# Performance work log

Measured on AMD Instinct MI355X. Metric: run time of the kernel, lower is better.

## Reference

```python
import jax, jax.numpy as jnp
import numpy as np

HEADS = 16
PHI = (1.0 + np.sqrt(5.0)) / 2.0


def setup_inputs() -> dict:
    key = jax.random.key(0)
    k1, k2, k3, k4 = jax.random.split(key, 4)
    B, L, D = 2, 2048, 1024
    x = jax.random.normal(k1, (B, L, D), dtype=jnp.float32)
    # nn.Linear(dim, 3*dim, bias=False): store as [D, 3D] for x @ W
    w_qkv = jax.random.normal(k2, (D, 3 * D), dtype=jnp.float32) * (D ** -0.5)
    w_proj = jax.random.normal(k3, (D, D), dtype=jnp.float32) * (D ** -0.5)
    b_proj = jax.random.normal(k4, (D,), dtype=jnp.float32) * 0.01
    return {"x": x, "w_qkv": w_qkv, "w_proj": w_proj, "b_proj": b_proj}


def phi_bias(L):
    # pos[i] = (i * phi) mod 1 ; bias = log(exp(-|pos_i - pos_j|) + 1e-8)
    pos = (jnp.arange(L, dtype=jnp.float32) * PHI) % 1.0
    dist = jnp.abs(pos[:, None] - pos[None, :])  # [L, L]
    return jnp.log(jnp.exp(-dist) + 1e-8)


def reference(x, w_qkv, w_proj, b_proj):
    B, L, D = x.shape
    H = HEADS
    Dh = D // H
    scale = Dh ** -0.5
    qkv = (x @ w_qkv).reshape(B, L, 3, H, Dh)
    q = jnp.transpose(qkv[:, :, 0], (0, 2, 1, 3))  # [B, H, L, Dh]
    k = jnp.transpose(qkv[:, :, 1], (0, 2, 1, 3))
    v = jnp.transpose(qkv[:, :, 2], (0, 2, 1, 3))
    attn = jnp.einsum("bhid,bhjd->bhij", q, k) * scale  # [B, H, L, L]
    attn = attn + phi_bias(L)[None, None]  # additive phi-distance bias
    attn = jax.nn.softmax(attn, axis=-1)
    out = jnp.einsum("bhij,bhjd->bhid", attn, v)  # [B, H, L, Dh]
    out = jnp.transpose(out, (0, 2, 1, 3)).reshape(B, L, D)
    return out @ w_proj + b_proj
```

## Files before the change

### kernel.cpp

```cpp
#include <hip/hip_runtime.h>
#include <math.h>


typedef _Float16 f16;
typedef _Float16 f16x4 __attribute__((ext_vector_type(4)));
typedef _Float16 f16x8 __attribute__((ext_vector_type(8)));
typedef float f32x4 __attribute__((ext_vector_type(4)));

#define MFMA32(a, b, c) __builtin_amdgcn_mfma_f32_16x16x32_f16(a, b, c, 0, 0, 0)

static constexpr int Bsz = 2, Lseq = 2048, Dm = 1024, H = 16, Dh = 64;
static constexpr int Mtot = Bsz * Lseq;
static constexpr int NQKV = 3 * Dm;
static constexpr float PHI_F = 1.61803398874989484820f;
static constexpr float LOG2E = 1.44269504088896f;
static constexpr float QS = 0.125f * LOG2E;
static constexpr float CSTEP = 0.55417527999932633f;

__device__ __forceinline__ void load16_to_lds(const f16* g, f16* l) {
  __builtin_amdgcn_global_load_lds(
      (const __attribute__((address_space(1))) unsigned int*)g,
      (__attribute__((address_space(3))) unsigned int*)l, 16, 0, 0);
}

__global__ __launch_bounds__(256) void cast_f32_f16(const float* __restrict__ in,
                                                    f16* __restrict__ out, int n) {
  int i = (blockIdx.x * 256 + threadIdx.x) * 4;
  if (i < n) {
    float4 v = *reinterpret_cast<const float4*>(in + i);
    f16 t[4] = {(f16)v.x, (f16)v.y, (f16)v.z, (f16)v.w};
    *reinterpret_cast<uint2*>(out + i) = *reinterpret_cast<uint2*>(t);
  }
}

__global__ __launch_bounds__(256) void transpose_cast(const float* __restrict__ in,
                                                      f16* __restrict__ out,
                                                      int K, int N) {
  __shared__ float tile[32][33];
  int n0 = blockIdx.x * 32, k0 = blockIdx.y * 32;
  int tx = threadIdx.x & 31, ty = threadIdx.x >> 5;
#pragma unroll
  for (int r = 0; r < 32; r += 8)
    tile[ty + r][tx] = in[(size_t)(k0 + ty + r) * N + n0 + tx];
  __syncthreads();
#pragma unroll
  for (int r = 0; r < 32; r += 8)
    out[(size_t)(n0 + ty + r) * K + k0 + tx] = (f16)tile[tx][ty + r];
}

__global__ __launch_bounds__(256) void v_transpose(const f16* __restrict__ in,
                                                   f16* __restrict__ out) {
  __shared__ f16 td[64][68];
  int bh = blockIdx.y, l0 = blockIdx.x * 64;
  int tid = threadIdx.x;
  const f16* src = in + (size_t)bh * Lseq * Dh;
#pragma unroll
  for (int c = tid; c < 512; c += 256) {
    int row = c >> 3, col = (c & 7) * 8;
    uint4 v = *reinterpret_cast<const uint4*>(src + (size_t)(l0 + row) * Dh + col);
    f16 tmp[8];
    *reinterpret_cast<uint4*>(tmp) = v;
#pragma unroll
    for (int j = 0; j < 8; j++) td[col + j][row] = tmp[j];
  }
  __syncthreads();
  f16* dst = out + (size_t)bh * Dh * Lseq;
#pragma unroll
  for (int c = tid; c < 512; c += 256) {
    int d = c >> 3, co = c & 7;
    int jh = co >> 2, qd = co & 3;
    f16 tmp[8];
#pragma unroll
    for (int e = 0; e < 4; e++) tmp[e] = td[d][jh * 32 + qd * 4 + e];
#pragma unroll
    for (int e = 0; e < 4; e++) tmp[4 + e] = td[d][jh * 32 + 16 + qd * 4 + e];
    *reinterpret_cast<uint4*>(dst + (size_t)d * Lseq + l0 + co * 8) =
        *reinterpret_cast<uint4*>(tmp);
  }
}

template <int MODE>
__global__ __launch_bounds__(256) void gemm_f16(
    const f16* __restrict__ A, const f16* __restrict__ Bt,
    int M, int N, int K,
    f16* __restrict__ qb, f16* __restrict__ kb, f16* __restrict__ vl,
    float* __restrict__ out, const float* __restrict__ bias) {
  constexpr int BM = (MODE == 0) ? 128 : 64;
  constexpr int MI = BM / 32;
  constexpr int AI = BM / 32;
  __shared__ f16 As[BM * 64];
  __shared__ f16 Bs[128 * 64];

  int tid = threadIdx.x;
  int wave = tid >> 6, lane = tid & 63;
  int quad = lane >> 4, l16 = lane & 15;
  int wm = (wave >> 1) * (MI * 16), wn = (wave & 1) * 64;

  int lid = blockIdx.x;
  int xcd = lid & 7, t = lid >> 3;
  int m0, n0;
  if (MODE == 0) {
    int mg = xcd >> 1, ng = xcd & 1;
    m0 = (mg * 8 + t / 12) * 128;
    n0 = (ng * 12 + t % 12) * 128;
  } else {
    m0 = (xcd * 8 + (t >> 3)) * 64;
    n0 = (t & 7) * 128;
  }

  const int gu = (lane & 7) ^ (lane >> 3);
  const f16* gA[AI];
  f16* lA[AI];
#pragma unroll
  for (int i = 0; i < AI; i++) {
    int it = wave * AI + i;
    gA[i] = A + (size_t)(m0 + it * 8 + (lane >> 3)) * K + gu * 8;
    lA[i] = As + it * 512;
  }
  const f16* gB[4];
  f16* lB[4];
#pragma unroll
  for (int i = 0; i < 4; i++) {
    int it = wave * 4 + i;
    gB[i] = Bt + (size_t)(n0 + it * 8 + (lane >> 3)) * K + gu * 8;
    lB[i] = Bs + it * 512;
  }

  f32x4 acc[MI][4] = {};

  for (int k0 = 0; k0 < K; k0 += 64) {
#pragma unroll
    for (int i = 0; i < AI; i++) load16_to_lds(gA[i] + k0, lA[i]);
#pragma unroll
    for (int i = 0; i < 4; i++) load16_to_lds(gB[i] + k0, lB[i]);
    __syncthreads();
#pragma unroll
    for (int s = 0; s < 2; s++) {
      f16x8 a[MI], b[4];
#pragma unroll
      for (int i = 0; i < MI; i++) {
        int row = wm + i * 16 + l16;
        a[i] = *reinterpret_cast<const f16x8*>(
            As + row * 64 + (((s * 4 + quad) ^ (l16 & 7)) * 8));
      }
#pragma unroll
      for (int j = 0; j < 4; j++) {
        int row = wn + j * 16 + l16;
        b[j] = *reinterpret_cast<const f16x8*>(
            Bs + row * 64 + (((s * 4 + quad) ^ (l16 & 7)) * 8));
      }
#pragma unroll
      for (int i = 0; i < MI; i++)
#pragma unroll
        for (int j = 0; j < 4; j++)
          acc[i][j] = MFMA32(a[i], b[j], acc[i][j]);
    }
    __syncthreads();
  }

#pragma unroll
  for (int i = 0; i < MI; i++) {
#pragma unroll
    for (int j = 0; j < 4; j++) {
      int n = n0 + wn + j * 16 + l16;
#pragma unroll
      for (int r = 0; r < 4; r++) {
        int m = m0 + wm + i * 16 + quad * 4 + r;
        if (MODE == 0) {
          int ty = n >> 10;
          int df = n & 1023;
          int h = df >> 6, dh = df & 63;
          int b = m >> 11, l = m & 2047;
          size_t idx = (((size_t)(b * H + h)) * Lseq + l) * Dh + dh;
          if (ty == 0)
            qb[idx] = (f16)(acc[i][j][r] * QS);
          else if (ty == 1)
            kb[idx] = (f16)acc[i][j][r];
          else
            vl[idx] = (f16)acc[i][j][r];
        } else {
          out[(size_t)m * N + n] = acc[i][j][r] + bias[n];
        }
      }
    }
  }
}

__global__ __launch_bounds__(256, 4) void attn_kernel(
    const f16* __restrict__ qb,
    const f16* __restrict__ kb,
    const f16* __restrict__ vb,
    f16* __restrict__ ctx) {
  __shared__ __align__(16) unsigned char smem[16640];
  f16* Ks = (f16*)smem;
  f16* Vs = (f16*)(smem + 8192);

  int bh = blockIdx.y;
  int q0 = blockIdx.x * 64;
  int tid = threadIdx.x, wave = tid >> 6, lane = tid & 63;
  int quad = lane >> 4, l16 = lane & 15;
  int jhalf = wave >> 1, qhalf = wave & 1;

  f16x8 qfrag[2][2];
  float pq[2];
#pragma unroll
  for (int set = 0; set < 2; set++) {
    int q = q0 + qhalf * 32 + set * 16 + l16;
    const f16* Qrow = qb + ((size_t)bh * Lseq + q) * Dh;
    qfrag[set][0] = *reinterpret_cast<const f16x8*>(Qrow + quad * 8);
    qfrag[set][1] = *reinterpret_cast<const f16x8*>(Qrow + 32 + quad * 8);
    pq[set] = fmodf((float)q * PHI_F, 1.0f);
  }

  float pk[2][4];
#pragma unroll
  for (int jb = 0; jb < 2; jb++)
#pragma unroll
    for (int r = 0; r < 4; r++) {
      int j = jhalf * 32 + jb * 16 + quad * 4 + r;
      pk[jb][r] = fmodf((float)j * PHI_F, 1.0f);
    }

  const f16* Kbh = kb + (size_t)bh * Lseq * Dh;
  const f16* Vbh = vb + (size_t)bh * Dh * Lseq;
  const int gu = (lane & 7) ^ (lane >> 3);
  const f16* gK[2];
  const f16* gV[2];
  f16* lK[2];
  f16* lV[2];
#pragma unroll
  for (int i = 0; i < 2; i++) {
    int g8 = (wave * 2 + i) * 8 + (lane >> 3);
    gK[i] = Kbh + (size_t)g8 * Dh + gu * 8;
    gV[i] = Vbh + (size_t)g8 * Lseq + gu * 8;
    lK[i] = Ks + (wave * 2 + i) * 512;
    lV[i] = Vs + (wave * 2 + i) * 512;
  }

  const f16 one = (f16)1.0f;
  const f16x8 ones8 = {one, one, one, one, one, one, one, one};

  f32x4 acc_o[2][4] = {};
  f32x4 acc_l[2] = {};

  for (int j0 = 0; j0 < Lseq; j0 += 64) {
    __syncthreads();
#pragma unroll
    for (int i = 0; i < 2; i++) {
      load16_to_lds(gK[i] + (size_t)j0 * Dh, lK[i]);
      load16_to_lds(gV[i] + j0, lV[i]);
    }
    __syncthreads();

    f32x4 accs[2][2] = {};
#pragma unroll
    for (int s = 0; s < 2; s++)
#pragma unroll
      for (int jb = 0; jb < 2; jb++) {
        f16x8 kf = *reinterpret_cast<const f16x8*>(
            Ks + (jhalf * 32 + jb * 16 + l16) * 64 + (((s * 4 + quad) ^ (l16 & 7)) * 8));
        accs[0][jb] = MFMA32(kf, qfrag[0][s], accs[0][jb]);
        accs[1][jb] = MFMA32(kf, qfrag[1][s], accs[1][jb]);
      }

    f16x8 pf8[2];
#pragma unroll
    for (int set = 0; set < 2; set++) {
#pragma unroll
      for (int jb = 0; jb < 2; jb++) {
        float p[4];
#pragma unroll
        for (int r = 0; r < 4; r++) {
          float d = pq[set] - pk[jb][r];
          float arg = fmaf(-LOG2E, fabsf(d), accs[set][jb][r]);
          p[r] = __builtin_amdgcn_exp2f(arg);
        }
        auto lo = __builtin_amdgcn_cvt_pkrtz(p[0], p[1]);
        auto hi = __builtin_amdgcn_cvt_pkrtz(p[2], p[3]);
        pf8[set][jb * 4 + 0] = lo[0];
        pf8[set][jb * 4 + 1] = lo[1];
        pf8[set][jb * 4 + 2] = hi[0];
        pf8[set][jb * 4 + 3] = hi[1];
      }
      acc_l[set] = MFMA32(ones8, pf8[set], acc_l[set]);
    }
#pragma unroll
    for (int jb = 0; jb < 2; jb++)
#pragma unroll
      for (int r = 0; r < 4; r++)
        pk[jb][r] = __builtin_amdgcn_fractf(pk[jb][r] + CSTEP);

#pragma unroll
    for (int dblk = 0; dblk < 4; dblk++) {
      int row = dblk * 16 + l16;
      f16x8 va = *reinterpret_cast<const f16x8*>(
          Vs + row * 64 + (((jhalf * 4 + quad) ^ (l16 & 7)) * 8));
      acc_o[0][dblk] = MFMA32(va, pf8[0], acc_o[0][dblk]);
      acc_o[1][dblk] = MFMA32(va, pf8[1], acc_o[1][dblk]);
    }
  }

  __syncthreads();
  float* Oex = (float*)smem;
  float* Lex = (float*)(smem + 16384);
  if (jhalf == 1) {
#pragma unroll
    for (int set = 0; set < 2; set++) {
#pragma unroll
      for (int dblk = 0; dblk < 4; dblk++)
#pragma unroll
        for (int r = 0; r < 4; r++)
          Oex[(((qhalf * 2 + set) * 4 + dblk) * 16 + quad * 4 + r) * 16 + l16] =
              acc_o[set][dblk][r];
      if (quad == 0) Lex[(qhalf * 2 + set) * 16 + l16] = acc_l[set][0];
    }
  }
  __syncthreads();
  if (jhalf == 0) {
    int b = bh >> 4, h = bh & 15;
#pragma unroll
    for (int set = 0; set < 2; set++) {
      float ltot = acc_l[set][0] + Lex[(qhalf * 2 + set) * 16 + l16];
      float inv = 1.0f / ltot;
      int q = q0 + qhalf * 32 + set * 16 + l16;
      f16* crow = ctx + (size_t)(b * Lseq + q) * Dm + h * 64;
#pragma unroll
      for (int dblk = 0; dblk < 4; dblk++) {
        f16x4 o;
#pragma unroll
        for (int r = 0; r < 4; r++) {
          float full = acc_o[set][dblk][r] +
              Oex[(((qhalf * 2 + set) * 4 + dblk) * 16 + quad * 4 + r) * 16 + l16];
          o[r] = (f16)(full * inv);
        }
        *reinterpret_cast<uint2*>(crow + dblk * 16 + quad * 4) =
            *reinterpret_cast<uint2*>(&o);
      }
    }
  }
}

extern "C" void kernel_launch(void* const* d_in, const int* in_sizes, int n_in,
                              void* d_out, int out_size, void* d_ws, size_t ws_size,
                              hipStream_t stream) {
  const float* x      = (const float*)d_in[0];
  const float* w_qkv  = (const float*)d_in[1];
  const float* w_proj = (const float*)d_in[2];
  const float* b_proj = (const float*)d_in[3];
  float* out = (float*)d_out;

  f16* xb    = (f16*)d_ws;
  f16* wqkvT = xb + (size_t)Mtot * Dm;
  f16* wpT   = wqkvT + (size_t)NQKV * Dm;
  f16* qb    = wpT + (size_t)Dm * Dm;
  f16* kb    = qb + (size_t)Bsz * H * Lseq * Dh;
  f16* vb    = kb + (size_t)Bsz * H * Lseq * Dh;
  f16* ctx   = vb + (size_t)Bsz * H * Lseq * Dh;
  f16* vl    = ctx;

  cast_f32_f16<<<(Mtot * Dm) / (256 * 4), 256, 0, stream>>>(x, xb, Mtot * Dm);
  transpose_cast<<<dim3(NQKV / 32, Dm / 32), 256, 0, stream>>>(w_qkv, wqkvT, Dm, NQKV);
  transpose_cast<<<dim3(Dm / 32, Dm / 32), 256, 0, stream>>>(w_proj, wpT, Dm, Dm);

  gemm_f16<0><<<768, 256, 0, stream>>>(
      xb, wqkvT, Mtot, NQKV, Dm, qb, kb, vl, nullptr, nullptr);

  v_transpose<<<dim3(Lseq / 64, Bsz * H), 256, 0, stream>>>(vl, vb);

  attn_kernel<<<dim3(Lseq / 64, Bsz * H), 256, 0, stream>>>(qb, kb, vb, ctx);

  gemm_f16<1><<<512, 256, 0, stream>>>(
      ctx, wpT, Mtot, Dm, Dm, nullptr, nullptr, nullptr, out, b_proj);
}
```

Baseline: 194.8 us.

## Double-buffer K/V tiles in attention with async LDS prefetch

```diff
diff --git a/kernel.cpp b/kernel.cpp
--- a/kernel.cpp
+++ b/kernel.cpp
@@ -21,6 +21,12 @@
   __builtin_amdgcn_global_load_lds(
       (const __attribute__((address_space(1))) unsigned int*)g,
       (__attribute__((address_space(3))) unsigned int*)l, 16, 0, 0);
+}
+
+__device__ __forceinline__ void barrier_fenced() {
+  __builtin_amdgcn_sched_barrier(0);
+  __builtin_amdgcn_s_barrier();
+  __builtin_amdgcn_sched_barrier(0);
 }
 
 __global__ __launch_bounds__(256) void cast_f32_f16(const float* __restrict__ in,
@@ -191,9 +197,9 @@
     const f16* __restrict__ kb,
     const f16* __restrict__ vb,
     f16* __restrict__ ctx) {
-  __shared__ __align__(16) unsigned char smem[16640];
+  __shared__ __align__(16) unsigned char smem[32768];
   f16* Ks = (f16*)smem;
-  f16* Vs = (f16*)(smem + 8192);
+  f16* Vs = (f16*)(smem + 16384);
 
   int bh = blockIdx.y;
   int q0 = blockIdx.x * 64;
@@ -243,25 +249,31 @@
   f32x4 acc_o[2][4] = {};
   f32x4 acc_l[2] = {};
 
-  for (int j0 = 0; j0 < Lseq; j0 += 64) {
-    __syncthreads();
+  auto stage = [&](int buf, int j0) __attribute__((always_inline)) {
 #pragma unroll
     for (int i = 0; i < 2; i++) {
-      load16_to_lds(gK[i] + (size_t)j0 * Dh, lK[i]);
-      load16_to_lds(gV[i] + j0, lV[i]);
-    }
-    __syncthreads();
+      load16_to_lds(gK[i] + (size_t)j0 * Dh, lK[i] + buf * 4096);
+      load16_to_lds(gV[i] + j0, lV[i] + buf * 4096);
+    }
+  };
+
+  auto compute = [&](int buf) __attribute__((always_inline)) {
+    const f16* Kc = Ks + buf * 4096;
+    const f16* Vc = Vs + buf * 4096;
 
     f32x4 accs[2][2] = {};
+    __builtin_amdgcn_s_setprio(1);
 #pragma unroll
     for (int s = 0; s < 2; s++)
 #pragma unroll
       for (int jb = 0; jb < 2; jb++) {
         f16x8 kf = *reinterpret_cast<const f16x8*>(
-            Ks + (jhalf * 32 + jb * 16 + l16) * 64 + (((s * 4 + quad) ^ (l16 & 7)) * 8));
+            Kc + (jhalf * 32 + jb * 16 + l16) * 64 +
+            (((s * 4 + quad) ^ (l16 & 7)) * 8));
         accs[0][jb] = MFMA32(kf, qfrag[0][s], accs[0][jb]);
         accs[1][jb] = MFMA32(kf, qfrag[1][s], accs[1][jb]);
       }
+    __builtin_amdgcn_s_setprio(0);
 
     f16x8 pf8[2];
 #pragma unroll
@@ -290,17 +302,36 @@
       for (int r = 0; r < 4; r++)
         pk[jb][r] = __builtin_amdgcn_fractf(pk[jb][r] + CSTEP);
 
+    __builtin_amdgcn_s_setprio(1);
 #pragma unroll
     for (int dblk = 0; dblk < 4; dblk++) {
       int row = dblk * 16 + l16;
       f16x8 va = *reinterpret_cast<const f16x8*>(
-          Vs + row * 64 + (((jhalf * 4 + quad) ^ (l16 & 7)) * 8));
+          Vc + row * 64 + (((jhalf * 4 + quad) ^ (l16 & 7)) * 8));
       acc_o[0][dblk] = MFMA32(va, pf8[0], acc_o[0][dblk]);
       acc_o[1][dblk] = MFMA32(va, pf8[1], acc_o[1][dblk]);
     }
-  }
-
-  __syncthreads();
+    __builtin_amdgcn_s_setprio(0);
+  };
+
+  stage(0, 0);
+#pragma unroll 1
+  for (int j0 = 0; j0 < Lseq; j0 += 128) {
+    stage(1, j0 + 64);
+    asm volatile("s_waitcnt vmcnt(4)" ::: "memory");
+    barrier_fenced();
+    compute(0);
+    barrier_fenced();
+    int jn = (j0 + 128 < Lseq) ? j0 + 128 : 0;
+    stage(0, jn);
+    asm volatile("s_waitcnt vmcnt(4)" ::: "memory");
+    barrier_fenced();
+    compute(1);
+    barrier_fenced();
+  }
+  asm volatile("s_waitcnt vmcnt(0)" ::: "memory");
+  barrier_fenced();
+
   float* Oex = (float*)smem;
   float* Lex = (float*)(smem + 16384);
   if (jhalf == 1) {
```

New measurement: 190.6 us. 2.2% less time.

## Split attention block across 8 waves with one 16-query set per wave

Applied to the files above, without the earlier changes.

```diff
diff --git a/kernel.cpp b/kernel.cpp
--- a/kernel.cpp
+++ b/kernel.cpp
@@ -16,6 +16,7 @@
 static constexpr float LOG2E = 1.44269504088896f;
 static constexpr float QS = 0.125f * LOG2E;
 static constexpr float CSTEP = 0.55417527999932633f;
+static constexpr float C16 = 0.88854381999831757f;
 
 __device__ __forceinline__ void load16_to_lds(const f16* g, f16* l) {
   __builtin_amdgcn_global_load_lds(
@@ -186,7 +187,7 @@
   }
 }
 
-__global__ __launch_bounds__(256, 4) void attn_kernel(
+__global__ __launch_bounds__(512, 8) void attn_kernel(
     const f16* __restrict__ qb,
     const f16* __restrict__ kb,
     const f16* __restrict__ vb,
@@ -199,105 +200,93 @@
   int q0 = blockIdx.x * 64;
   int tid = threadIdx.x, wave = tid >> 6, lane = tid & 63;
   int quad = lane >> 4, l16 = lane & 15;
-  int jhalf = wave >> 1, qhalf = wave & 1;
-
-  f16x8 qfrag[2][2];
-  float pq[2];
-#pragma unroll
-  for (int set = 0; set < 2; set++) {
-    int q = q0 + qhalf * 32 + set * 16 + l16;
-    const f16* Qrow = qb + ((size_t)bh * Lseq + q) * Dh;
-    qfrag[set][0] = *reinterpret_cast<const f16x8*>(Qrow + quad * 8);
-    qfrag[set][1] = *reinterpret_cast<const f16x8*>(Qrow + 32 + quad * 8);
-    pq[set] = fmodf((float)q * PHI_F, 1.0f);
-  }
-
-  float pk[2][4];
-#pragma unroll
-  for (int jb = 0; jb < 2; jb++)
-#pragma unroll
-    for (int r = 0; r < 4; r++) {
-      int j = jhalf * 32 + jb * 16 + quad * 4 + r;
-      pk[jb][r] = fmodf((float)j * PHI_F, 1.0f);
-    }
-
-  const f16* Kbh = kb + (size_t)bh * Lseq * Dh;
-  const f16* Vbh = vb + (size_t)bh * Dh * Lseq;
+  int jhalf = wave >> 2, qq = wave & 3;
+
+  int q = q0 + qq * 16 + l16;
+  const f16* Qrow = qb + ((size_t)bh * Lseq + q) * Dh;
+  f16x8 qfrag0 = *reinterpret_cast<const f16x8*>(Qrow + quad * 8);
+  f16x8 qfrag1 = *reinterpret_cast<const f16x8*>(Qrow + 32 + quad * 8);
+  float pq = fmodf((float)q * PHI_F, 1.0f);
+
+  float pk0[4];
+#pragma unroll
+  for (int r = 0; r < 4; r++) {
+    int j = jhalf * 32 + quad * 4 + r;
+    pk0[r] = fmodf((float)j * PHI_F, 1.0f);
+  }
+
   const int gu = (lane & 7) ^ (lane >> 3);
-  const f16* gK[2];
-  const f16* gV[2];
-  f16* lK[2];
-  f16* lV[2];
-#pragma unroll
-  for (int i = 0; i < 2; i++) {
-    int g8 = (wave * 2 + i) * 8 + (lane >> 3);
-    gK[i] = Kbh + (size_t)g8 * Dh + gu * 8;
-    gV[i] = Vbh + (size_t)g8 * Lseq + gu * 8;
-    lK[i] = Ks + (wave * 2 + i) * 512;
-    lV[i] = Vs + (wave * 2 + i) * 512;
-  }
+  int g8 = wave * 8 + (lane >> 3);
+  const f16* gK = kb + (size_t)bh * Lseq * Dh + (size_t)g8 * Dh + gu * 8;
+  const f16* gV = vb + (size_t)bh * Dh * Lseq + (size_t)g8 * Lseq + gu * 8;
+  f16* lK = Ks + wave * 512;
+  f16* lV = Vs + wave * 512;
 
   const f16 one = (f16)1.0f;
   const f16x8 ones8 = {one, one, one, one, one, one, one, one};
 
-  f32x4 acc_o[2][4] = {};
-  f32x4 acc_l[2] = {};
-
+  f32x4 acc_o[4] = {};
+  f32x4 acc_l = {};
+
+  const f16* kfp0 = Ks + (jhalf * 32 + l16) * 64 + ((quad ^ (l16 & 7)) * 8);
+  const f16* kfp1 = Ks + (jhalf * 32 + l16) * 64 + (((4 + quad) ^ (l16 & 7)) * 8);
+  const f16* vfp = Vs + l16 * 64 + (((jhalf * 4 + quad) ^ (l16 & 7)) * 8);
+
+#pragma unroll 1
   for (int j0 = 0; j0 < Lseq; j0 += 64) {
     __syncthreads();
-#pragma unroll
-    for (int i = 0; i < 2; i++) {
-      load16_to_lds(gK[i] + (size_t)j0 * Dh, lK[i]);
-      load16_to_lds(gV[i] + j0, lV[i]);
-    }
+    load16_to_lds(gK + (size_t)j0 * Dh, lK);
+    load16_to_lds(gV + j0, lV);
     __syncthreads();
 
-    f32x4 accs[2][2] = {};
-#pragma unroll
-    for (int s = 0; s < 2; s++)
-#pragma unroll
-      for (int jb = 0; jb < 2; jb++) {
-        f16x8 kf = *reinterpret_cast<const f16x8*>(
-            Ks + (jhalf * 32 + jb * 16 + l16) * 64 + (((s * 4 + quad) ^ (l16 & 7)) * 8));
-        accs[0][jb] = MFMA32(kf, qfrag[0][s], accs[0][jb]);
-        accs[1][jb] = MFMA32(kf, qfrag[1][s], accs[1][jb]);
-      }
-
-    f16x8 pf8[2];
-#pragma unroll
-    for (int set = 0; set < 2; set++) {
-#pragma unroll
-      for (int jb = 0; jb < 2; jb++) {
-        float p[4];
-#pragma unroll
-        for (int r = 0; r < 4; r++) {
-          float d = pq[set] - pk[jb][r];
-          float arg = fmaf(-LOG2E, fabsf(d), accs[set][jb][r]);
-          p[r] = __builtin_amdgcn_exp2f(arg);
-        }
-        auto lo = __builtin_amdgcn_cvt_pkrtz(p[0], p[1]);
-        auto hi = __builtin_amdgcn_cvt_pkrtz(p[2], p[3]);
-        pf8[set][jb * 4 + 0] = lo[0];
-        pf8[set][jb * 4 + 1] = lo[1];
-        pf8[set][jb * 4 + 2] = hi[0];
-        pf8[set][jb * 4 + 3] = hi[1];
-      }
-      acc_l[set] = MFMA32(ones8, pf8[set], acc_l[set]);
-    }
-#pragma unroll
-    for (int jb = 0; jb < 2; jb++)
-#pragma unroll
-      for (int r = 0; r < 4; r++)
-        pk[jb][r] = __builtin_amdgcn_fractf(pk[jb][r] + CSTEP);
-
+    f32x4 accs[2];
+    float pk1[4];
+#pragma unroll
+    for (int r = 0; r < 4; r++) {
+      accs[0][r] = -LOG2E * fabsf(pq - pk0[r]);
+      pk1[r] = __builtin_amdgcn_fractf(pk0[r] + C16);
+    }
+#pragma unroll
+    for (int r = 0; r < 4; r++) {
+      accs[1][r] = -LOG2E * fabsf(pq - pk1[r]);
+      pk0[r] = __builtin_amdgcn_fractf(pk0[r] + CSTEP);
+    }
+
+    __builtin_amdgcn_s_setprio(1);
+    {
+      f16x8 kf00 = *reinterpret_cast<const f16x8*>(kfp0);
+      f16x8 kf01 = *reinterpret_cast<const f16x8*>(kfp1);
+      f16x8 kf10 = *reinterpret_cast<const f16x8*>(kfp0 + 16 * 64);
+      f16x8 kf11 = *reinterpret_cast<const f16x8*>(kfp1 + 16 * 64);
+      accs[0] = MFMA32(kf00, qfrag0, accs[0]);
+      accs[0] = MFMA32(kf01, qfrag1, accs[0]);
+      accs[1] = MFMA32(kf10, qfrag0, accs[1]);
+      accs[1] = MFMA32(kf11, qfrag1, accs[1]);
+    }
+    __builtin_amdgcn_s_setprio(0);
+
+    f16x8 pf8;
+#pragma unroll
+    for (int jb = 0; jb < 2; jb++) {
+      float p[4];
+#pragma unroll
+      for (int r = 0; r < 4; r++) p[r] = __builtin_amdgcn_exp2f(accs[jb][r]);
+      auto lo = __builtin_amdgcn_cvt_pkrtz(p[0], p[1]);
+      auto hi = __builtin_amdgcn_cvt_pkrtz(p[2], p[3]);
+      pf8[jb * 4 + 0] = lo[0];
+      pf8[jb * 4 + 1] = lo[1];
+      pf8[jb * 4 + 2] = hi[0];
+      pf8[jb * 4 + 3] = hi[1];
+    }
+    acc_l = MFMA32(ones8, pf8, acc_l);
+
+    __builtin_amdgcn_s_setprio(1);
 #pragma unroll
     for (int dblk = 0; dblk < 4; dblk++) {
-      int row = dblk * 16 + l16;
-      f16x8 va = *reinterpret_cast<const f16x8*>(
-          Vs + row * 64 + (((jhalf * 4 + quad) ^ (l16 & 7)) * 8));
-      acc_o[0][dblk] = MFMA32(va, pf8[0], acc_o[0][dblk]);
-      acc_o[1][dblk] = MFMA32(va, pf8[1], acc_o[1][dblk]);
-    }
+      f16x8 va = *reinterpret_cast<const f16x8*>(vfp + dblk * 16 * 64);
+      acc_o[dblk] = MFMA32(va, pf8, acc_o[dblk]);
+    }
+    __builtin_amdgcn_s_setprio(0);
   }
 
   __syncthreads();
@@ -305,37 +294,29 @@
   float* Lex = (float*)(smem + 16384);
   if (jhalf == 1) {
 #pragma unroll
-    for (int set = 0; set < 2; set++) {
-#pragma unroll
-      for (int dblk = 0; dblk < 4; dblk++)
-#pragma unroll
-        for (int r = 0; r < 4; r++)
-          Oex[(((qhalf * 2 + set) * 4 + dblk) * 16 + quad * 4 + r) * 16 + l16] =
-              acc_o[set][dblk][r];
-      if (quad == 0) Lex[(qhalf * 2 + set) * 16 + l16] = acc_l[set][0];
-    }
+    for (int dblk = 0; dblk < 4; dblk++)
+#pragma unroll
+      for (int r = 0; r < 4; r++)
+        Oex[((qq * 4 + dblk) * 16 + quad * 4 + r) * 16 + l16] = acc_o[dblk][r];
+    if (quad == 0) Lex[qq * 16 + l16] = acc_l[0];
   }
   __syncthreads();
   if (jhalf == 0) {
     int b = bh >> 4, h = bh & 15;
-#pragma unroll
-    for (int set = 0; set < 2; set++) {
-      float ltot = acc_l[set][0] + Lex[(qhalf * 2 + set) * 16 + l16];
-      float inv = 1.0f / ltot;
-      int q = q0 + qhalf * 32 + set * 16 + l16;
-      f16* crow = ctx + (size_t)(b * Lseq + q) * Dm + h * 64;
-#pragma unroll
-      for (int dblk = 0; dblk < 4; dblk++) {
-        f16x4 o;
-#pragma unroll
-        for (int r = 0; r < 4; r++) {
-          float full = acc_o[set][dblk][r] +
-              Oex[(((qhalf * 2 + set) * 4 + dblk) * 16 + quad * 4 + r) * 16 + l16];
-          o[r] = (f16)(full * inv);
-        }
-        *reinterpret_cast<uint2*>(crow + dblk * 16 + quad * 4) =
-            *reinterpret_cast<uint2*>(&o);
+    float ltot = acc_l[0] + Lex[qq * 16 + l16];
+    float inv = 1.0f / ltot;
+    f16* crow = ctx + (size_t)(b * Lseq + q) * Dm + h * 64;
+#pragma unroll
+    for (int dblk = 0; dblk < 4; dblk++) {
+      f16x4 o;
+#pragma unroll
+      for (int r = 0; r < 4; r++) {
+        float full = acc_o[dblk][r] +
+            Oex[((qq * 4 + dblk) * 16 + quad * 4 + r) * 16 + l16];
+        o[r] = (f16)(full * inv);
       }
+      *reinterpret_cast<uint2*>(crow + dblk * 16 + quad * 4) =
+          *reinterpret_cast<uint2*>(&o);
     }
   }
 }
@@ -367,7 +348,7 @@
 
   v_transpose<<<dim3(Lseq / 64, Bsz * H), 256, 0, stream>>>(vl, vb);
 
-  attn_kernel<<<dim3(Lseq / 64, Bsz * H), 256, 0, stream>>>(qb, kb, vb, ctx);
+  attn_kernel<<<dim3(Lseq / 64, Bsz * H), 512, 0, stream>>>(qb, kb, vb, ctx);
 
   gemm_f16<1><<<512, 256, 0, stream>>>(
       ctx, wpT, Mtot, Dm, Dm, nullptr, nullptr, nullptr, out, b_proj);
```

New measurement: 206.6 us. 1.06x slower.

## Give each wave private K/V LDS buffers with blocked V layout, removing block barriers

Applied to the files above, without the earlier changes.

```diff
diff --git a/kernel.cpp b/kernel.cpp
--- a/kernel.cpp
+++ b/kernel.cpp
@@ -64,7 +64,7 @@
     for (int j = 0; j < 8; j++) td[col + j][row] = tmp[j];
   }
   __syncthreads();
-  f16* dst = out + (size_t)bh * Dh * Lseq;
+  f16* dst = out + (size_t)bh * Dh * Lseq + (size_t)(l0 >> 6) * 4096;
 #pragma unroll
   for (int c = tid; c < 512; c += 256) {
     int d = c >> 3, co = c & 7;
@@ -74,7 +74,7 @@
     for (int e = 0; e < 4; e++) tmp[e] = td[d][jh * 32 + qd * 4 + e];
 #pragma unroll
     for (int e = 0; e < 4; e++) tmp[4 + e] = td[d][jh * 32 + 16 + qd * 4 + e];
-    *reinterpret_cast<uint4*>(dst + (size_t)d * Lseq + l0 + co * 8) =
+    *reinterpret_cast<uint4*>(dst + d * 64 + co * 8) =
         *reinterpret_cast<uint4*>(tmp);
   }
 }
@@ -191,15 +191,16 @@
     const f16* __restrict__ kb,
     const f16* __restrict__ vb,
     f16* __restrict__ ctx) {
-  __shared__ __align__(16) unsigned char smem[16640];
-  f16* Ks = (f16*)smem;
-  f16* Vs = (f16*)(smem + 8192);
+  __shared__ __align__(16) unsigned char smem[32768];
 
   int bh = blockIdx.y;
   int q0 = blockIdx.x * 64;
   int tid = threadIdx.x, wave = tid >> 6, lane = tid & 63;
   int quad = lane >> 4, l16 = lane & 15;
   int jhalf = wave >> 1, qhalf = wave & 1;
+
+  f16* Kp = (f16*)(smem + wave * 8192);
+  f16* Vp = (f16*)(smem + wave * 8192 + 4096);
 
   f16x8 qfrag[2][2];
   float pq[2];
@@ -223,19 +224,26 @@
 
   const f16* Kbh = kb + (size_t)bh * Lseq * Dh;
   const f16* Vbh = vb + (size_t)bh * Dh * Lseq;
-  const int gu = (lane & 7) ^ (lane >> 3);
-  const f16* gK[2];
-  const f16* gV[2];
-  f16* lK[2];
-  f16* lV[2];
-#pragma unroll
-  for (int i = 0; i < 2; i++) {
-    int g8 = (wave * 2 + i) * 8 + (lane >> 3);
-    gK[i] = Kbh + (size_t)g8 * Dh + gu * 8;
-    gV[i] = Vbh + (size_t)g8 * Lseq + gu * 8;
-    lK[i] = Ks + (wave * 2 + i) * 512;
-    lV[i] = Vs + (wave * 2 + i) * 512;
-  }
+  const f16* gK[4];
+  f16* lK[4];
+  const int gu8 = (lane & 7) ^ (lane >> 3);
+#pragma unroll
+  for (int i = 0; i < 4; i++) {
+    gK[i] = Kbh + (size_t)(jhalf * 32 + i * 8 + (lane >> 3)) * 64 + gu8 * 8;
+    lK[i] = Kp + i * 512;
+  }
+  const f16* gV[4];
+  f16* lV[4];
+  const int gu4 = (lane & 3) ^ ((lane >> 3) & 3);
+#pragma unroll
+  for (int i = 0; i < 4; i++) {
+    gV[i] = Vbh + (size_t)(i * 16 + (lane >> 2)) * 64 + (jhalf * 4 + gu4) * 8;
+    lV[i] = Vp + i * 512;
+  }
+
+  const f16* kfp0 = Kp + l16 * 64 + ((quad ^ (l16 & 7)) * 8);
+  const f16* kfp1 = Kp + l16 * 64 + (((4 + quad) ^ (l16 & 7)) * 8);
+  const f16* vfp = Vp + l16 * 32 + ((quad ^ ((l16 >> 1) & 3)) * 8);
 
   const f16 one = (f16)1.0f;
   const f16x8 ones8 = {one, one, one, one, one, one, one, one};
@@ -243,25 +251,46 @@
   f32x4 acc_o[2][4] = {};
   f32x4 acc_l[2] = {};
 
-  for (int j0 = 0; j0 < Lseq; j0 += 64) {
-    __syncthreads();
-#pragma unroll
-    for (int i = 0; i < 2; i++) {
-      load16_to_lds(gK[i] + (size_t)j0 * Dh, lK[i]);
-      load16_to_lds(gV[i] + j0, lV[i]);
-    }
-    __syncthreads();
-
-    f32x4 accs[2][2] = {};
-#pragma unroll
-    for (int s = 0; s < 2; s++)
-#pragma unroll
-      for (int jb = 0; jb < 2; jb++) {
-        f16x8 kf = *reinterpret_cast<const f16x8*>(
-            Ks + (jhalf * 32 + jb * 16 + l16) * 64 + (((s * 4 + quad) ^ (l16 & 7)) * 8));
-        accs[0][jb] = MFMA32(kf, qfrag[0][s], accs[0][jb]);
-        accs[1][jb] = MFMA32(kf, qfrag[1][s], accs[1][jb]);
-      }
+#pragma unroll
+  for (int i = 0; i < 4; i++) load16_to_lds(gK[i], lK[i]);
+#pragma unroll
+  for (int i = 0; i < 4; i++) load16_to_lds(gV[i], lV[i]);
+#pragma unroll
+  for (int i = 0; i < 4; i++) { gK[i] += 4096; gV[i] += 4096; }
+
+#pragma unroll 1
+  for (int t = 0; t < 32; ++t) {
+    asm volatile("s_waitcnt vmcnt(4)" ::: "memory");
+    __builtin_amdgcn_sched_barrier(0);
+    f16x8 kf00 = *reinterpret_cast<const f16x8*>(kfp0);
+    f16x8 kf10 = *reinterpret_cast<const f16x8*>(kfp1);
+    f16x8 kf01 = *reinterpret_cast<const f16x8*>(kfp0 + 1024);
+    f16x8 kf11 = *reinterpret_cast<const f16x8*>(kfp1 + 1024);
+    asm volatile("s_waitcnt lgkmcnt(0)" ::: "memory");
+    __builtin_amdgcn_sched_barrier(0);
+#pragma unroll
+    for (int i = 0; i < 4; i++) load16_to_lds(gK[i], lK[i]);
+    __builtin_amdgcn_sched_barrier(0);
+
+    f32x4 accs[2][2];
+#pragma unroll
+    for (int jb = 0; jb < 2; jb++)
+#pragma unroll
+      for (int r = 0; r < 4; r++) {
+        accs[0][jb][r] = -LOG2E * fabsf(pq[0] - pk[jb][r]);
+        accs[1][jb][r] = -LOG2E * fabsf(pq[1] - pk[jb][r]);
+        pk[jb][r] = __builtin_amdgcn_fractf(pk[jb][r] + CSTEP);
+      }
+
+    __builtin_amdgcn_s_setprio(1);
+#pragma unroll
+    for (int set = 0; set < 2; set++) {
+      accs[set][0] = MFMA32(kf00, qfrag[set][0], accs[set][0]);
+      accs[set][0] = MFMA32(kf10, qfrag[set][1], accs[set][0]);
+      accs[set][1] = MFMA32(kf01, qfrag[set][0], accs[set][1]);
+      accs[set][1] = MFMA32(kf11, qfrag[set][1], accs[set][1]);
+    }
+    __builtin_amdgcn_s_setprio(0);
 
     f16x8 pf8[2];
 #pragma unroll
@@ -270,11 +299,8 @@
       for (int jb = 0; jb < 2; jb++) {
         float p[4];
 #pragma unroll
-        for (int r = 0; r < 4; r++) {
-          float d = pq[set] - pk[jb][r];
-          float arg = fmaf(-LOG2E, fabsf(d), accs[set][jb][r]);
-          p[r] = __builtin_amdgcn_exp2f(arg);
-        }
+        for (int r = 0; r < 4; r++)
+          p[r] = __builtin_amdgcn_exp2f(accs[set][jb][r]);
         auto lo = __builtin_amdgcn_cvt_pkrtz(p[0], p[1]);
         auto hi = __builtin_amdgcn_cvt_pkrtz(p[2], p[3]);
         pf8[set][jb * 4 + 0] = lo[0];
@@ -284,23 +310,35 @@
       }
       acc_l[set] = MFMA32(ones8, pf8[set], acc_l[set]);
     }
-#pragma unroll
-    for (int jb = 0; jb < 2; jb++)
-#pragma unroll
-      for (int r = 0; r < 4; r++)
-        pk[jb][r] = __builtin_amdgcn_fractf(pk[jb][r] + CSTEP);
-
-#pragma unroll
-    for (int dblk = 0; dblk < 4; dblk++) {
-      int row = dblk * 16 + l16;
-      f16x8 va = *reinterpret_cast<const f16x8*>(
-          Vs + row * 64 + (((jhalf * 4 + quad) ^ (l16 & 7)) * 8));
-      acc_o[0][dblk] = MFMA32(va, pf8[0], acc_o[0][dblk]);
-      acc_o[1][dblk] = MFMA32(va, pf8[1], acc_o[1][dblk]);
-    }
-  }
-
+
+    asm volatile("s_waitcnt vmcnt(4)" ::: "memory");
+    __builtin_amdgcn_sched_barrier(0);
+    f16x8 va0 = *reinterpret_cast<const f16x8*>(vfp);
+    f16x8 va1 = *reinterpret_cast<const f16x8*>(vfp + 512);
+    f16x8 va2 = *reinterpret_cast<const f16x8*>(vfp + 1024);
+    f16x8 va3 = *reinterpret_cast<const f16x8*>(vfp + 1536);
+    asm volatile("s_waitcnt lgkmcnt(0)" ::: "memory");
+    __builtin_amdgcn_sched_barrier(0);
+#pragma unroll
+    for (int i = 0; i < 4; i++) load16_to_lds(gV[i], lV[i]);
+    __builtin_amdgcn_sched_barrier(0);
+#pragma unroll
+    for (int i = 0; i < 4; i++) { gK[i] += 4096; gV[i] += 4096; }
+
+    __builtin_amdgcn_s_setprio(1);
+    acc_o[0][0] = MFMA32(va0, pf8[0], acc_o[0][0]);
+    acc_o[1][0] = MFMA32(va0, pf8[1], acc_o[1][0]);
+    acc_o[0][1] = MFMA32(va1, pf8[0], acc_o[0][1]);
+    acc_o[1][1] = MFMA32(va1, pf8[1], acc_o[1][1]);
+    acc_o[0][2] = MFMA32(va2, pf8[0], acc_o[0][2]);
+    acc_o[1][2] = MFMA32(va2, pf8[1], acc_o[1][2]);
+    acc_o[0][3] = MFMA32(va3, pf8[0], acc_o[0][3]);
+    acc_o[1][3] = MFMA32(va3, pf8[1], acc_o[1][3]);
+    __builtin_amdgcn_s_setprio(0);
+  }
+  asm volatile("s_waitcnt vmcnt(0)" ::: "memory");
   __syncthreads();
+
   float* Oex = (float*)smem;
   float* Lex = (float*)(smem + 16384);
   if (jhalf == 1) {
```

New measurement: 240.7 us. 23.5% more time.
